# Optimization experiments

Measured on AMD Instinct MI355X. Metric: run time of the kernel, lower is better.

The kernel has to match this reference:

```python
import jax, jax.numpy as jnp
import numpy as np

B, T, L = 32, 512, 16   # clips, transitions per clip, IMU samples per transition
C_IN = 6
H1, H2, H3 = 64, 128, 256
OUT = 256
EPS = 1e-5
SLOPE = 0.1


def setup_inputs() -> dict:
    key = jax.random.key(0)
    ks = jax.random.split(key, 24)
    f32 = jnp.float32

    def n(k, shape, s=0.05):
        return jax.random.normal(k, shape, f32) * s

    inp = {
        "imu": jax.random.normal(ks[0], (B, T, L, C_IN), f32),
        # conv block 1
        "w1": n(ks[1], (H1, C_IN, 3)), "b1": n(ks[2], (H1,)),
        "g1": 1.0 + n(ks[3], (H1,)), "be1": n(ks[4], (H1,)),
        "m1": n(ks[5], (H1,)), "v1": jax.random.uniform(ks[6], (H1,), f32, 0.5, 1.5),
        # conv block 2
        "w2": n(ks[7], (H2, H1, 3)), "b2": n(ks[8], (H2,)),
        "g2": 1.0 + n(ks[9], (H2,)), "be2": n(ks[10], (H2,)),
        "m2": n(ks[11], (H2,)), "v2": jax.random.uniform(ks[12], (H2,), f32, 0.5, 1.5),
        # conv block 3
        "w3": n(ks[13], (H3, H2, 3)), "b3": n(ks[14], (H3,)),
        "g3": 1.0 + n(ks[15], (H3,)), "be3": n(ks[16], (H3,)),
        "m3": n(ks[17], (H3,)), "v3": jax.random.uniform(ks[18], (H3,), f32, 0.5, 1.5),
        # projection (torch Linear: y = x @ W.T + b)
        "wp": n(ks[19], (OUT, H3)), "bp": n(ks[20], (OUT,)),
    }
    return inp


def _conv1d(x, w, b):
    # x: [N, C, L], w: [O, I, K], 'same' padding=1 for K=3
    y = jax.lax.conv_general_dilated(
        x, w, window_strides=(1,), padding=[(1, 1)],
        dimension_numbers=("NCH", "OIH", "NCH"))
    return y + b[None, :, None]


def _block(x, w, b, g, be, m, v):
    # Conv1d -> BatchNorm1d (eval, running stats) -> LeakyReLU(0.1); dropout = identity (eval)
    y = _conv1d(x, w, b)
    y = g[None, :, None] * (y - m[None, :, None]) * jax.lax.rsqrt(v + EPS)[None, :, None] + be[None, :, None]
    return jnp.where(y > 0, y, SLOPE * y)


def reference(imu, w1, b1, g1, be1, m1, v1,
              w2, b2, g2, be2, m2, v2,
              w3, b3, g3, be3, m3, v3,
              wp, bp):
    # Flatten the (batch, transition) double loop into one batched pipeline.
    # imu: [B, T, L, 6] -> [B*T, 6, L]  (= .transpose(0,1).unsqueeze(0) per segment)
    x = imu.reshape(B * T, L, C_IN).transpose(0, 2, 1)
    x = _block(x, w1, b1, g1, be1, m1, v1)
    x = _block(x, w2, b2, g2, be2, m2, v2)
    x = _block(x, w3, b3, g3, be3, m3, v3)   # [B*T, 256, L]
    x = jnp.mean(x, axis=-1)                  # AdaptiveAvgPool1d(1) -> [B*T, 256]
    out = x @ wp.T + bp                       # projection -> [B*T, 256]
    return out.reshape(B, T, OUT)
```

## Files before the change

kernel.cpp:

```cpp
#include <hip/hip_runtime.h>
#include <cstdint>
#include <cstddef>


namespace {

typedef __attribute__((ext_vector_type(8))) short short8;
typedef __attribute__((ext_vector_type(4))) float f32x4;

constexpr int NSEG = 32 * 512;
constexpr float kEps = 1e-5f;

constexpr size_t OFF_A2F = 0;
constexpr size_t OFF_A3F = 49152;
constexpr size_t OFF_WP  = 245760;
constexpr size_t OFF_B2  = 376832;
constexpr size_t OFF_B3  = 377344;
constexpr size_t OFF_A1F = 378368;
constexpr size_t OFF_B1C = 382464;
constexpr size_t WS_NEED = 382720;

constexpr int L_ACT2 = 20736;
constexpr int L_IMC  = 59904;
constexpr int L_POOL = 70144;
constexpr int L_TOTAL = 78592;

__device__ __forceinline__ unsigned short f2bf(float f) {
    union { float f; unsigned int u; } a; a.f = f;
    unsigned int u = a.u + 0x7FFFu + ((a.u >> 16) & 1u);
    return (unsigned short)(u >> 16);
}

__device__ __forceinline__ unsigned int cvt_pk_bf16(float a, float b) {
    unsigned int r;
    asm("v_cvt_pk_bf16_f32 %0, %1, %2" : "=v"(r) : "v"(a), "v"(b));
    return r;
}
__device__ __forceinline__ float asf(unsigned int u) {
    union { unsigned int u; float f; } a; a.u = u; return a.f;
}

__device__ __forceinline__ void gll16(const void* g, void* l) {
    __builtin_amdgcn_global_load_lds(
        (const __attribute__((address_space(1))) unsigned int*)g,
        (__attribute__((address_space(3))) unsigned int*)l, 16, 0, 0);
}

__device__ __forceinline__ short8 frag16(const void* p) {
    return __builtin_bit_cast(short8, *(const int4*)p);
}

__device__ __forceinline__ void sync_lds() {
    asm volatile("s_waitcnt lgkmcnt(0)" ::: "memory");
    __builtin_amdgcn_s_barrier();
    asm volatile("" ::: "memory");
    __builtin_amdgcn_sched_barrier(0);
}
__device__ __forceinline__ void sync_vm_lds() {
    asm volatile("s_waitcnt vmcnt(0) lgkmcnt(0)" ::: "memory");
    __builtin_amdgcn_s_barrier();
    asm volatile("" ::: "memory");
    __builtin_amdgcn_sched_barrier(0);
}

__device__ __forceinline__ float leaky(float y) { return fmaxf(y, 0.1f * y); }

__global__ __launch_bounds__(256) void k0_prep(
    const float* __restrict__ w1, const float* __restrict__ b1, const float* __restrict__ g1,
    const float* __restrict__ be1, const float* __restrict__ m1, const float* __restrict__ v1,
    const float* __restrict__ w2, const float* __restrict__ b2, const float* __restrict__ g2,
    const float* __restrict__ be2, const float* __restrict__ m2, const float* __restrict__ v2,
    const float* __restrict__ w3, const float* __restrict__ b3, const float* __restrict__ g3,
    const float* __restrict__ be3, const float* __restrict__ m3, const float* __restrict__ v3,
    const float* __restrict__ wp, char* __restrict__ ws)
{
    int idx = blockIdx.x * 256 + threadIdx.x;
    if (idx < 3072) {
        int f = idx >> 6, lane = idx & 63;
        int tap = f >> 4, qq = (f >> 3) & 1, rtile = f & 7;
        int row = rtile * 16 + (lane & 15);
        int kb = qq * 32 + (lane >> 4) * 8;
        float a = g2[row] * rsqrtf(v2[row] + kEps);
        unsigned short us[8];
#pragma unroll
        for (int j = 0; j < 8; ++j)
            us[j] = f2bf(a * w2[row * 192 + (kb + j) * 3 + tap]);
        *(int4*)(ws + OFF_A2F + (size_t)idx * 16) = *(const int4*)us;
    } else if (idx < 15360) {
        int u = idx - 3072;
        int f = u >> 6, lane = u & 63;
        int ks = f >> 5, qq = (f >> 4) & 1, rtile = f & 15;
        int tap = ks >> 1, ih = ks & 1;
        int row = rtile * 16 + (lane & 15);
        int kb = qq * 32 + (lane >> 4) * 8;
        float a = g3[row] * rsqrtf(v3[row] + kEps);
        unsigned short us[8];
#pragma unroll
        for (int j = 0; j < 8; ++j) {
            int i = ih * 64 + kb + j;
            us[j] = f2bf(a * w3[row * 384 + i * 3 + tap]);
        }
        *(int4*)(ws + OFF_A3F + (size_t)u * 16) = *(const int4*)us;
    } else if (idx < 23552) {
        int u = idx - 15360;
        int f = u >> 6, lane = u & 63;
        int o = (f >> 3) * 16 + (lane & 15);
        int cb = (f & 7) * 32 + (lane >> 4) * 8;
        unsigned short us[8];
#pragma unroll
        for (int j = 0; j < 8; ++j)
            us[j] = f2bf(wp[o * 256 + cb + j] * 0.0625f);
        *(int4*)(ws + OFF_WP + (size_t)u * 16) = *(const int4*)us;
    } else if (idx < 23680) {
        int o = idx - 23552;
        float a = g2[o] * rsqrtf(v2[o] + kEps);
        ((float*)(ws + OFF_B2))[o] = a * (b2[o] - m2[o]) + be2[o];
    } else if (idx < 23936) {
        int o = idx - 23680;
        float a = g3[o] * rsqrtf(v3[o] + kEps);
        ((float*)(ws + OFF_B3))[o] = a * (b3[o] - m3[o]) + be3[o];
    } else if (idx < 24192) {
        int u = idx - 23936;
        int f = u >> 6, lane = u & 63;
        int row = f * 16 + (lane & 15);
        float a = g1[row] * rsqrtf(v1[row] + kEps);
        unsigned short us[8];
#pragma unroll
        for (int j = 0; j < 8; ++j) {
            int k = (lane >> 4) * 8 + j;
            us[j] = (k < 18) ? f2bf(a * w1[row * 18 + k]) : (unsigned short)0;
        }
        *(int4*)(ws + OFF_A1F + (size_t)u * 16) = *(const int4*)us;
    } else if (idx < 24256) {
        int o = idx - 24192;
        float a = g1[o] * rsqrtf(v1[o] + kEps);
        ((float*)(ws + OFF_B1C))[o] = a * (b1[o] - m1[o]) + be1[o];
    }
}

__global__ __launch_bounds__(512, 4) void k_all(
    const float* __restrict__ imu,
    const char* __restrict__ ws, const float* __restrict__ bp,
    float* __restrict__ out)
{
    __shared__ char smem[L_TOTAL];
    char* act1L  = smem;
    char* act2L  = smem + L_ACT2;
    char* imcL   = smem + L_IMC;
    char* poolsL = smem + L_POOL;
    char* imuL   = poolsL;
    const char* A2F = ws + OFF_A2F;
    const char* A3F = ws + OFF_A3F;
    const char* WPF = ws + OFF_WP;
    const float* bias2 = (const float*)(ws + OFF_B2);
    const float* bias3 = (const float*)(ws + OFF_B3);

    const int tid = threadIdx.x, lane = tid & 63, wid = tid >> 6;
    const int lo = lane & 15, hi = lane >> 4;
    const int seg0 = blockIdx.x * 8;

    short8 a1p[4];
#pragma unroll
    for (int m = 0; m < 4; ++m)
        a1p[m] = frag16(ws + OFF_A1F + (size_t)(m * 64 + lane) * 16);
    float4 bb4[4];
#pragma unroll
    for (int m = 0; m < 4; ++m)
        bb4[m] = *(const float4*)((const float*)(ws + OFF_B1C) + m * 16 + hi * 4);

    if (wid < 3)
        gll16((const char*)imu + (size_t)seg0 * 384 + wid * 1024 + lane * 16,
              imuL + wid * 1024);
    sync_vm_lds();

    {
        const float* xf = (const float*)imuL;
        const int kq = wid & 3;
        const int col = (wid >> 2) * 64 + lane;
        const int seg = col >> 4, l = col & 15;
        const float* xb = xf + seg * 96 + l * 6;
        float v[8];
        if (kq == 0) {
            v[0] = l > 0  ? xb[-6] : 0.f;
            v[1] = xb[0];
            v[2] = l < 15 ? xb[6]  : 0.f;
            v[3] = l > 0  ? xb[-5] : 0.f;
            v[4] = xb[1];
            v[5] = l < 15 ? xb[7]  : 0.f;
            v[6] = l > 0  ? xb[-4] : 0.f;
            v[7] = xb[2];
        } else if (kq == 1) {
            v[0] = l < 15 ? xb[8]  : 0.f;
            v[1] = l > 0  ? xb[-3] : 0.f;
            v[2] = xb[3];
            v[3] = l < 15 ? xb[9]  : 0.f;
            v[4] = l > 0  ? xb[-2] : 0.f;
            v[5] = xb[4];
            v[6] = l < 15 ? xb[10] : 0.f;
            v[7] = l > 0  ? xb[-1] : 0.f;
        } else if (kq == 2) {
            v[0] = xb[5];
            v[1] = l < 15 ? xb[11] : 0.f;
            v[2] = v[3] = v[4] = v[5] = v[6] = v[7] = 0.f;
        } else {
            v[0] = v[1] = v[2] = v[3] = v[4] = v[5] = v[6] = v[7] = 0.f;
        }
        uint4 pk;
        pk.x = cvt_pk_bf16(v[0], v[1]);
        pk.y = cvt_pk_bf16(v[2], v[3]);
        pk.z = cvt_pk_bf16(v[4], v[5]);
        pk.w = cvt_pk_bf16(v[6], v[7]);
        *(uint4*)(imcL + seg * 1280 + l * 80 + kq * 16) = pk;

        if (tid < 144) {
            int s = tid / 18, rest = tid % 18;
            int h = rest / 9, unit = rest % 9;
            int4 z; z.x = z.y = z.z = z.w = 0;
            *(int4*)(act1L + (s * 18 + h * 17) * 144 + unit * 16) = z;
        }
        if (tid < 272) {
            int s = tid / 34, rest = tid % 34;
            int h = rest / 17, unit = rest % 17;
            int4 z; z.x = z.y = z.z = z.w = 0;
            *(int4*)(act2L + (s * 18 + h * 17) * 272 + unit * 16) = z;
        }
    }
    sync_lds();

    {
        f32x4 acc1[4];
#pragma unroll
        for (int m = 0; m < 4; ++m) acc1[m] = f32x4{0.f, 0.f, 0.f, 0.f};
        short8 bq = frag16(imcL + wid * 1280 + lo * 80 + hi * 16);
        __builtin_amdgcn_s_setprio(1);
#pragma unroll
        for (int m = 0; m < 4; ++m)
            acc1[m] = __builtin_amdgcn_mfma_f32_16x16x32_bf16(a1p[m], bq, acc1[m], 0, 0, 0);
        __builtin_amdgcn_s_setprio(0);
#pragma unroll
        for (int m = 0; m < 4; ++m) {
            float y0 = leaky(acc1[m][0] + bb4[m].x);
            float y1 = leaky(acc1[m][1] + bb4[m].y);
            float y2 = leaky(acc1[m][2] + bb4[m].z);
            float y3 = leaky(acc1[m][3] + bb4[m].w);
            uint2 pk;
            pk.x = cvt_pk_bf16(y0, y1);
            pk.y = cvt_pk_bf16(y2, y3);
            *(uint2*)(act1L + (wid * 18 + lo + 1) * 144 + m * 32 + hi * 8) = pk;
        }
    }

    const int mi2 = wid >> 1, ni2 = wid & 1;
    short8 a2p[2][2];
#pragma unroll
    for (int s = 0; s < 2; ++s)
#pragma unroll
        for (int rt = 0; rt < 2; ++rt)
            a2p[s][rt] = frag16(A2F + (size_t)((s * 8 + mi2 * 2 + rt) * 64 + lane) * 16);

    sync_lds();

    f32x4 acc2[2][4];
#pragma unroll
    for (int i = 0; i < 2; ++i)
#pragma unroll
        for (int j = 0; j < 4; ++j) acc2[i][j] = f32x4{0.f, 0.f, 0.f, 0.f};
    {
        const char* b1base = act1L + lo * 144 + hi * 16;
#pragma unroll
        for (int s = 0; s < 6; ++s) {
            const int tap = s >> 1, qq = s & 1;
            short8 bfr[4];
#pragma unroll
            for (int ct = 0; ct < 4; ++ct)
                bfr[ct] = frag16(b1base + ((ni2 * 4 + ct) * 18 + tap) * 144 + qq * 64);
            __builtin_amdgcn_s_setprio(1);
#pragma unroll
            for (int ct = 0; ct < 4; ++ct) {
                acc2[0][ct] = __builtin_amdgcn_mfma_f32_16x16x32_bf16(a2p[s & 1][0], bfr[ct], acc2[0][ct], 0, 0, 0);
                acc2[1][ct] = __builtin_amdgcn_mfma_f32_16x16x32_bf16(a2p[s & 1][1], bfr[ct], acc2[1][ct], 0, 0, 0);
            }
            __builtin_amdgcn_s_setprio(0);
            if (s < 4) {
#pragma unroll
                for (int rt = 0; rt < 2; ++rt)
                    a2p[s & 1][rt] = frag16(A2F + (size_t)(((s + 2) * 8 + mi2 * 2 + rt) * 64 + lane) * 16);
            }
        }
    }

    const int ni3 = wid >> 1, mi3 = wid & 1;
    short8 w3p[2][4];
#pragma unroll
    for (int s = 0; s < 2; ++s)
#pragma unroll
        for (int ct = 0; ct < 4; ++ct)
            w3p[s][ct] = frag16(A3F + (size_t)((s * 16 + ni3 * 4 + ct) * 64 + lane) * 16);
    float b3r[4];
#pragma unroll
    for (int ct = 0; ct < 4; ++ct)
        b3r[ct] = bias3[(ni3 * 4 + ct) * 16 + lo];

#pragma unroll
    for (int rt = 0; rt < 2; ++rt) {
        int ch0 = (mi2 * 2 + rt) * 16 + hi * 4;
        float4 b4 = *(const float4*)(bias2 + ch0);
#pragma unroll
        for (int ct = 0; ct < 4; ++ct) {
            float y0 = leaky(acc2[rt][ct][0] + b4.x);
            float y1 = leaky(acc2[rt][ct][1] + b4.y);
            float y2 = leaky(acc2[rt][ct][2] + b4.z);
            float y3 = leaky(acc2[rt][ct][3] + b4.w);
            uint2 pk;
            pk.x = cvt_pk_bf16(y0, y1);
            pk.y = cvt_pk_bf16(y2, y3);
            *(uint2*)(act2L + ((ni2 * 4 + ct) * 18 + lo + 1) * 272 + ch0 * 2) = pk;
        }
    }
    sync_lds();

    f32x4 acc3[4][4];
#pragma unroll
    for (int i = 0; i < 4; ++i)
#pragma unroll
        for (int j = 0; j < 4; ++j) acc3[i][j] = f32x4{0.f, 0.f, 0.f, 0.f};
    {
#pragma unroll
        for (int s = 0; s < 12; ++s) {
            const int tap = s >> 2, ih = (s >> 1) & 1, qq = s & 1;
            short8 afr[4];
#pragma unroll
            for (int mt = 0; mt < 4; ++mt)
                afr[mt] = frag16(act2L + ((mi3 * 4 + mt) * 18 + lo + tap) * 272
                                 + ih * 128 + qq * 64 + hi * 16);
            __builtin_amdgcn_s_setprio(1);
#pragma unroll
            for (int mt = 0; mt < 4; ++mt)
#pragma unroll
                for (int ct = 0; ct < 4; ++ct)
                    acc3[mt][ct] = __builtin_amdgcn_mfma_f32_16x16x32_bf16(
                        afr[mt], w3p[s & 1][ct], acc3[mt][ct], 0, 0, 0);
            __builtin_amdgcn_s_setprio(0);
            if (s < 10) {
#pragma unroll
                for (int ct = 0; ct < 4; ++ct)
                    w3p[s & 1][ct] = frag16(A3F + (size_t)(((s + 2) * 16 + ni3 * 4 + ct) * 64 + lane) * 16);
            }
        }
    }

#pragma unroll
    for (int ct = 0; ct < 4; ++ct) {
        int co = (ni3 * 4 + ct) * 16 + lo;
        float bv = b3r[ct];
        float t[4];
#pragma unroll
        for (int mt = 0; mt < 4; ++mt) {
            float s4 = 0.f;
#pragma unroll
            for (int r = 0; r < 4; ++r)
                s4 += leaky(acc3[mt][ct][r] + bv);
            s4 += __shfl_xor(s4, 16, 64);
            s4 += __shfl_xor(s4, 32, 64);
            t[mt] = s4;
        }
        unsigned int pkA = cvt_pk_bf16(t[0], t[1]);
        unsigned int pkB = cvt_pk_bf16(t[2], t[3]);
        float r0 = t[0] - asf(pkA << 16);
        float r1 = t[1] - asf(pkA & 0xffff0000u);
        float r2 = t[2] - asf(pkB << 16);
        float r3 = t[3] - asf(pkB & 0xffff0000u);
        unsigned int pkrA = cvt_pk_bf16(r0, r1);
        unsigned int pkrB = cvt_pk_bf16(r2, r3);
        if (hi == 0) {
            int row0 = mi3 * 4;
            char* pc = poolsL + co * 2;
            *(unsigned short*)(pc + (row0 + 0) * 528) = (unsigned short)pkA;
            *(unsigned short*)(pc + (row0 + 1) * 528) = (unsigned short)(pkA >> 16);
            *(unsigned short*)(pc + (row0 + 2) * 528) = (unsigned short)pkB;
            *(unsigned short*)(pc + (row0 + 3) * 528) = (unsigned short)(pkB >> 16);
            *(unsigned short*)(pc + (row0 + 8) * 528) = (unsigned short)pkrA;
            *(unsigned short*)(pc + (row0 + 9) * 528) = (unsigned short)(pkrA >> 16);
            *(unsigned short*)(pc + (row0 + 10) * 528) = (unsigned short)pkrB;
            *(unsigned short*)(pc + (row0 + 11) * 528) = (unsigned short)(pkrB >> 16);
        }
    }

    short8 wbp[2][2];
#pragma unroll
    for (int q = 0; q < 2; ++q)
#pragma unroll
        for (int ct = 0; ct < 2; ++ct)
            wbp[q][ct] = frag16(WPF + (size_t)(((wid * 2 + ct) * 8 + q) * 64 + lane) * 16);

    sync_lds();

    {
        f32x4 acc4[2];
        acc4[0] = f32x4{0.f, 0.f, 0.f, 0.f};
        acc4[1] = f32x4{0.f, 0.f, 0.f, 0.f};
#pragma unroll
        for (int q = 0; q < 8; ++q) {
            short8 pa = frag16(poolsL + lo * 528 + q * 64 + hi * 16);
            acc4[0] = __builtin_amdgcn_mfma_f32_16x16x32_bf16(pa, wbp[q & 1][0], acc4[0], 0, 0, 0);
            acc4[1] = __builtin_amdgcn_mfma_f32_16x16x32_bf16(pa, wbp[q & 1][1], acc4[1], 0, 0, 0);
            if (q < 6) {
#pragma unroll
                for (int ct = 0; ct < 2; ++ct)
                    wbp[q & 1][ct] = frag16(WPF + (size_t)(((wid * 2 + ct) * 8 + q + 2) * 64 + lane) * 16);
            }
        }
#pragma unroll
        for (int ct = 0; ct < 2; ++ct) {
            int o = (wid * 2 + ct) * 16 + lo;
            float bv = bp[o];
#pragma unroll
            for (int r = 0; r < 4; ++r) {
                float t = acc4[ct][r] + __shfl_xor(acc4[ct][r], 32, 64);
                if (hi < 2)
                    out[(size_t)(seg0 + hi * 4 + r) * 256 + o] = t + bv;
            }
        }
    }
}

}

extern "C" void kernel_launch(void* const* d_in, const int* in_sizes, int n_in,
                              void* d_out, int out_size, void* d_ws, size_t ws_size,
                              hipStream_t stream) {
    if (ws_size < WS_NEED) return;

    const float* imu = (const float*)d_in[0];
    const float* w1 = (const float*)d_in[1];  const float* b1 = (const float*)d_in[2];
    const float* g1 = (const float*)d_in[3];  const float* be1 = (const float*)d_in[4];
    const float* m1 = (const float*)d_in[5];  const float* v1 = (const float*)d_in[6];
    const float* w2 = (const float*)d_in[7];  const float* b2 = (const float*)d_in[8];
    const float* g2 = (const float*)d_in[9];  const float* be2 = (const float*)d_in[10];
    const float* m2 = (const float*)d_in[11]; const float* v2 = (const float*)d_in[12];
    const float* w3 = (const float*)d_in[13]; const float* b3 = (const float*)d_in[14];
    const float* g3 = (const float*)d_in[15]; const float* be3 = (const float*)d_in[16];
    const float* m3 = (const float*)d_in[17]; const float* v3 = (const float*)d_in[18];
    const float* wp = (const float*)d_in[19]; const float* bp = (const float*)d_in[20];
    float* out = (float*)d_out;
    char* ws = (char*)d_ws;

    hipLaunchKernelGGL(k0_prep, dim3(95), dim3(256), 0, stream,
                       w1, b1, g1, be1, m1, v1,
                       w2, b2, g2, be2, m2, v2, w3, b3, g3, be3, m3, v3, wp, ws);
    hipLaunchKernelGGL(k_all, dim3(NSEG / 8), dim3(512), 0, stream,
                       imu, ws, bp, out);
}
```

Before: 82.03 us.

## Switch layer-3 conv GEMM to 32x32x16 MFMA with re-tiled weight fragments

Layer 3 moves from 16x16x32 bf16 MFMAs to 32x32x16 bf16 MFMAs. The layer-3 weight prepack layout is rearranged to match, and the wave-to-tile mapping becomes two segments by 128 output channels per wave. This cuts the number of LDS activation fragment loads per MFMA and issues fewer, larger matrix instructions, aiming at higher matrix-core throughput. In exchange, the accumulators move into 16-wide vectors, which may change register pressure, and the pooling epilogue and its LDS writes are rewritten for the new accumulator layout.

```diff
diff --git a/kernel.cpp b/kernel.cpp
--- a/kernel.cpp
+++ b/kernel.cpp
@@ -7,6 +7,7 @@
 
 typedef __attribute__((ext_vector_type(8))) short short8;
 typedef __attribute__((ext_vector_type(4))) float f32x4;
+typedef __attribute__((ext_vector_type(16))) float f32x16;
 
 constexpr int NSEG = 32 * 512;
 constexpr float kEps = 1e-5f;
@@ -89,16 +90,16 @@
     } else if (idx < 15360) {
         int u = idx - 3072;
         int f = u >> 6, lane = u & 63;
-        int ks = f >> 5, qq = (f >> 4) & 1, rtile = f & 15;
-        int tap = ks >> 1, ih = ks & 1;
-        int row = rtile * 16 + (lane & 15);
-        int kb = qq * 32 + (lane >> 4) * 8;
-        float a = g3[row] * rsqrtf(v3[row] + kEps);
+        int ks = f >> 3, ctile = f & 7;
+        int tap = ks >> 3;
+        int cout = ctile * 32 + (lane & 31);
+        int klocal = (lane >> 5) * 8;
+        float a = g3[cout] * rsqrtf(v3[cout] + kEps);
         unsigned short us[8];
 #pragma unroll
         for (int j = 0; j < 8; ++j) {
-            int i = ih * 64 + kb + j;
-            us[j] = f2bf(a * w3[row * 384 + i * 3 + tap]);
+            int i = (ks & 7) * 16 + klocal + j;
+            us[j] = f2bf(a * w3[cout * 384 + i * 3 + tap]);
         }
         *(int4*)(ws + OFF_A3F + (size_t)u * 16) = *(const int4*)us;
     } else if (idx < 23552) {
@@ -289,17 +290,18 @@
         }
     }
 
-    const int ni3 = wid >> 1, mi3 = wid & 1;
+    const int s0 = 2 * (wid & 3);
+    const int cb32 = (wid >> 2) * 4;
     short8 w3p[2][4];
 #pragma unroll
     for (int s = 0; s < 2; ++s)
 #pragma unroll
         for (int ct = 0; ct < 4; ++ct)
-            w3p[s][ct] = frag16(A3F + (size_t)((s * 16 + ni3 * 4 + ct) * 64 + lane) * 16);
+            w3p[s][ct] = frag16(A3F + (size_t)((s * 8 + cb32 + ct) * 64 + lane) * 16);
     float b3r[4];
 #pragma unroll
     for (int ct = 0; ct < 4; ++ct)
-        b3r[ct] = bias3[(ni3 * 4 + ct) * 16 + lo];
+        b3r[ct] = bias3[(cb32 + ct) * 32 + (lane & 31)];
 
 #pragma unroll
     for (int rt = 0; rt < 2; ++rt) {
@@ -319,70 +321,56 @@
     }
     sync_lds();
 
-    f32x4 acc3[4][4];
-#pragma unroll
-    for (int i = 0; i < 4; ++i)
-#pragma unroll
-        for (int j = 0; j < 4; ++j) acc3[i][j] = f32x4{0.f, 0.f, 0.f, 0.f};
+    f32x16 acc3v[4];
+#pragma unroll
+    for (int t = 0; t < 4; ++t)
+#pragma unroll
+        for (int r = 0; r < 16; ++r) acc3v[t][r] = 0.f;
     {
-#pragma unroll
-        for (int s = 0; s < 12; ++s) {
-            const int tap = s >> 2, ih = (s >> 1) & 1, qq = s & 1;
-            short8 afr[4];
-#pragma unroll
-            for (int mt = 0; mt < 4; ++mt)
-                afr[mt] = frag16(act2L + ((mi3 * 4 + mt) * 18 + lo + tap) * 272
-                                 + ih * 128 + qq * 64 + hi * 16);
+        const int arow = lane & 31;
+        const char* a3base = act2L + ((s0 + (arow >> 4)) * 18 + (arow & 15)) * 272
+                             + (lane >> 5) * 16;
+#pragma unroll
+        for (int ks = 0; ks < 24; ++ks) {
+            const int tap = ks >> 3, kc = ks & 7;
+            short8 afr = frag16(a3base + tap * 272 + kc * 32);
             __builtin_amdgcn_s_setprio(1);
 #pragma unroll
-            for (int mt = 0; mt < 4; ++mt)
+            for (int t = 0; t < 4; ++t)
+                acc3v[t] = __builtin_amdgcn_mfma_f32_32x32x16_bf16(
+                    afr, w3p[ks & 1][t], acc3v[t], 0, 0, 0);
+            __builtin_amdgcn_s_setprio(0);
+            if (ks < 22) {
 #pragma unroll
                 for (int ct = 0; ct < 4; ++ct)
-                    acc3[mt][ct] = __builtin_amdgcn_mfma_f32_16x16x32_bf16(
-                        afr[mt], w3p[s & 1][ct], acc3[mt][ct], 0, 0, 0);
-            __builtin_amdgcn_s_setprio(0);
-            if (s < 10) {
-#pragma unroll
-                for (int ct = 0; ct < 4; ++ct)
-                    w3p[s & 1][ct] = frag16(A3F + (size_t)(((s + 2) * 16 + ni3 * 4 + ct) * 64 + lane) * 16);
+                    w3p[ks & 1][ct] = frag16(A3F + (size_t)(((ks + 2) * 8 + cb32 + ct) * 64 + lane) * 16);
             }
         }
     }
 
 #pragma unroll
-    for (int ct = 0; ct < 4; ++ct) {
-        int co = (ni3 * 4 + ct) * 16 + lo;
-        float bv = b3r[ct];
-        float t[4];
-#pragma unroll
-        for (int mt = 0; mt < 4; ++mt) {
-            float s4 = 0.f;
-#pragma unroll
-            for (int r = 0; r < 4; ++r)
-                s4 += leaky(acc3[mt][ct][r] + bv);
-            s4 += __shfl_xor(s4, 16, 64);
-            s4 += __shfl_xor(s4, 32, 64);
-            t[mt] = s4;
-        }
-        unsigned int pkA = cvt_pk_bf16(t[0], t[1]);
-        unsigned int pkB = cvt_pk_bf16(t[2], t[3]);
-        float r0 = t[0] - asf(pkA << 16);
-        float r1 = t[1] - asf(pkA & 0xffff0000u);
-        float r2 = t[2] - asf(pkB << 16);
-        float r3 = t[3] - asf(pkB & 0xffff0000u);
-        unsigned int pkrA = cvt_pk_bf16(r0, r1);
-        unsigned int pkrB = cvt_pk_bf16(r2, r3);
-        if (hi == 0) {
-            int row0 = mi3 * 4;
-            char* pc = poolsL + co * 2;
-            *(unsigned short*)(pc + (row0 + 0) * 528) = (unsigned short)pkA;
-            *(unsigned short*)(pc + (row0 + 1) * 528) = (unsigned short)(pkA >> 16);
-            *(unsigned short*)(pc + (row0 + 2) * 528) = (unsigned short)pkB;
-            *(unsigned short*)(pc + (row0 + 3) * 528) = (unsigned short)(pkB >> 16);
-            *(unsigned short*)(pc + (row0 + 8) * 528) = (unsigned short)pkrA;
-            *(unsigned short*)(pc + (row0 + 9) * 528) = (unsigned short)(pkrA >> 16);
-            *(unsigned short*)(pc + (row0 + 10) * 528) = (unsigned short)pkrB;
-            *(unsigned short*)(pc + (row0 + 11) * 528) = (unsigned short)(pkrB >> 16);
+    for (int t = 0; t < 4; ++t) {
+        float bv = b3r[t];
+        float sA = 0.f, sB = 0.f;
+#pragma unroll
+        for (int r = 0; r < 8; ++r)
+            sA += leaky(acc3v[t][r] + bv);
+#pragma unroll
+        for (int r = 8; r < 16; ++r)
+            sB += leaky(acc3v[t][r] + bv);
+        sA += __shfl_xor(sA, 32, 64);
+        sB += __shfl_xor(sB, 32, 64);
+        unsigned int pk = cvt_pk_bf16(sA, sB);
+        float rA = sA - asf(pk << 16);
+        float rB = sB - asf(pk & 0xffff0000u);
+        unsigned int pkr = cvt_pk_bf16(rA, rB);
+        if (lane < 32) {
+            int cout = (cb32 + t) * 32 + lane;
+            char* pc = poolsL + cout * 2;
+            *(unsigned short*)(pc + (s0 + 0) * 528) = (unsigned short)pk;
+            *(unsigned short*)(pc + (s0 + 1) * 528) = (unsigned short)(pk >> 16);
+            *(unsigned short*)(pc + (s0 + 8) * 528) = (unsigned short)pkr;
+            *(unsigned short*)(pc + (s0 + 9) * 528) = (unsigned short)(pkr >> 16);
         }
     }
 
```

Result: slower. 88.37 us (+7.7%).

## Build layer-1 im2col fragments in registers and drop staging barriers

Applied to the files above, without the earlier changes.

Each wave now loads its own segment's IMU data into a private LDS slice and waits only on its own vector loads, with no block barrier. It then builds the layer-1 MFMA B-fragment directly in registers instead of staging an im2col buffer in LDS. This removes two block-wide barriers and one LDS round trip, and frees about 10 KB of LDS per block. The s_setprio hints around the MFMA loops are also removed. The halo zeroing of act1/act2 moves after layer 1, and the LDS region holding the raw IMU data is reused for pooling later, so correctness depends on the remaining barrier ordering.

```diff
diff --git a/kernel.cpp b/kernel.cpp
--- a/kernel.cpp
+++ b/kernel.cpp
@@ -21,9 +21,8 @@
 constexpr size_t WS_NEED = 382720;
 
 constexpr int L_ACT2 = 20736;
-constexpr int L_IMC  = 59904;
-constexpr int L_POOL = 70144;
-constexpr int L_TOTAL = 78592;
+constexpr int L_POOL = 59904;
+constexpr int L_TOTAL = 68352;
 
 __device__ __forceinline__ unsigned short f2bf(float f) {
     union { float f; unsigned int u; } a; a.f = f;
@@ -52,12 +51,6 @@
 
 __device__ __forceinline__ void sync_lds() {
     asm volatile("s_waitcnt lgkmcnt(0)" ::: "memory");
-    __builtin_amdgcn_s_barrier();
-    asm volatile("" ::: "memory");
-    __builtin_amdgcn_sched_barrier(0);
-}
-__device__ __forceinline__ void sync_vm_lds() {
-    asm volatile("s_waitcnt vmcnt(0) lgkmcnt(0)" ::: "memory");
     __builtin_amdgcn_s_barrier();
     asm volatile("" ::: "memory");
     __builtin_amdgcn_sched_barrier(0);
@@ -146,7 +139,6 @@
     __shared__ char smem[L_TOTAL];
     char* act1L  = smem;
     char* act2L  = smem + L_ACT2;
-    char* imcL   = smem + L_IMC;
     char* poolsL = smem + L_POOL;
     char* imuL   = poolsL;
     const char* A2F = ws + OFF_A2F;
@@ -168,75 +160,53 @@
     for (int m = 0; m < 4; ++m)
         bb4[m] = *(const float4*)((const float*)(ws + OFF_B1C) + m * 16 + hi * 4);
 
-    if (wid < 3)
-        gll16((const char*)imu + (size_t)seg0 * 384 + wid * 1024 + lane * 16,
-              imuL + wid * 1024);
-    sync_vm_lds();
+    if (lane < 24)
+        gll16((const char*)imu + (size_t)(seg0 + wid) * 384 + lane * 16,
+              imuL + wid * 384);
+    asm volatile("s_waitcnt vmcnt(0)" ::: "memory");
+    __builtin_amdgcn_sched_barrier(0);
 
     {
-        const float* xf = (const float*)imuL;
-        const int kq = wid & 3;
-        const int col = (wid >> 2) * 64 + lane;
-        const int seg = col >> 4, l = col & 15;
-        const float* xb = xf + seg * 96 + l * 6;
+        const float* xb = (const float*)(imuL + wid * 384) + lo * 6;
         float v[8];
-        if (kq == 0) {
-            v[0] = l > 0  ? xb[-6] : 0.f;
+        if (hi == 0) {
+            v[0] = lo > 0  ? xb[-6] : 0.f;
             v[1] = xb[0];
-            v[2] = l < 15 ? xb[6]  : 0.f;
-            v[3] = l > 0  ? xb[-5] : 0.f;
+            v[2] = lo < 15 ? xb[6]  : 0.f;
+            v[3] = lo > 0  ? xb[-5] : 0.f;
             v[4] = xb[1];
-            v[5] = l < 15 ? xb[7]  : 0.f;
-            v[6] = l > 0  ? xb[-4] : 0.f;
+            v[5] = lo < 15 ? xb[7]  : 0.f;
+            v[6] = lo > 0  ? xb[-4] : 0.f;
             v[7] = xb[2];
-        } else if (kq == 1) {
-            v[0] = l < 15 ? xb[8]  : 0.f;
-            v[1] = l > 0  ? xb[-3] : 0.f;
+        } else if (hi == 1) {
+            v[0] = lo < 15 ? xb[8]  : 0.f;
+            v[1] = lo > 0  ? xb[-3] : 0.f;
             v[2] = xb[3];
-            v[3] = l < 15 ? xb[9]  : 0.f;
-            v[4] = l > 0  ? xb[-2] : 0.f;
+            v[3] = lo < 15 ? xb[9]  : 0.f;
+            v[4] = lo > 0  ? xb[-2] : 0.f;
             v[5] = xb[4];
-            v[6] = l < 15 ? xb[10] : 0.f;
-            v[7] = l > 0  ? xb[-1] : 0.f;
-        } else if (kq == 2) {
+            v[6] = lo < 15 ? xb[10] : 0.f;
+            v[7] = lo > 0  ? xb[-1] : 0.f;
+        } else if (hi == 2) {
             v[0] = xb[5];
-            v[1] = l < 15 ? xb[11] : 0.f;
+            v[1] = lo < 15 ? xb[11] : 0.f;
             v[2] = v[3] = v[4] = v[5] = v[6] = v[7] = 0.f;
         } else {
             v[0] = v[1] = v[2] = v[3] = v[4] = v[5] = v[6] = v[7] = 0.f;
         }
-        uint4 pk;
-        pk.x = cvt_pk_bf16(v[0], v[1]);
-        pk.y = cvt_pk_bf16(v[2], v[3]);
-        pk.z = cvt_pk_bf16(v[4], v[5]);
-        pk.w = cvt_pk_bf16(v[6], v[7]);
-        *(uint4*)(imcL + seg * 1280 + l * 80 + kq * 16) = pk;
-
-        if (tid < 144) {
-            int s = tid / 18, rest = tid % 18;
-            int h = rest / 9, unit = rest % 9;
-            int4 z; z.x = z.y = z.z = z.w = 0;
-            *(int4*)(act1L + (s * 18 + h * 17) * 144 + unit * 16) = z;
-        }
-        if (tid < 272) {
-            int s = tid / 34, rest = tid % 34;
-            int h = rest / 17, unit = rest % 17;
-            int4 z; z.x = z.y = z.z = z.w = 0;
-            *(int4*)(act2L + (s * 18 + h * 17) * 272 + unit * 16) = z;
-        }
-    }
-    sync_lds();
-
-    {
+        uint4 pkv;
+        pkv.x = cvt_pk_bf16(v[0], v[1]);
+        pkv.y = cvt_pk_bf16(v[2], v[3]);
+        pkv.z = cvt_pk_bf16(v[4], v[5]);
+        pkv.w = cvt_pk_bf16(v[6], v[7]);
+        short8 bq = __builtin_bit_cast(short8, pkv);
+
         f32x4 acc1[4];
 #pragma unroll
         for (int m = 0; m < 4; ++m) acc1[m] = f32x4{0.f, 0.f, 0.f, 0.f};
-        short8 bq = frag16(imcL + wid * 1280 + lo * 80 + hi * 16);
-        __builtin_amdgcn_s_setprio(1);
 #pragma unroll
         for (int m = 0; m < 4; ++m)
             acc1[m] = __builtin_amdgcn_mfma_f32_16x16x32_bf16(a1p[m], bq, acc1[m], 0, 0, 0);
-        __builtin_amdgcn_s_setprio(0);
 #pragma unroll
         for (int m = 0; m < 4; ++m) {
             float y0 = leaky(acc1[m][0] + bb4[m].x);
@@ -248,6 +218,18 @@
             pk.y = cvt_pk_bf16(y2, y3);
             *(uint2*)(act1L + (wid * 18 + lo + 1) * 144 + m * 32 + hi * 8) = pk;
         }
+        if (tid < 144) {
+            int s = tid / 18, rest = tid % 18;
+            int h = rest / 9, unit = rest % 9;
+            int4 z; z.x = z.y = z.z = z.w = 0;
+            *(int4*)(act1L + (s * 18 + h * 17) * 144 + unit * 16) = z;
+        }
+        if (tid < 272) {
+            int s = tid / 34, rest = tid % 34;
+            int h = rest / 17, unit = rest % 17;
+            int4 z; z.x = z.y = z.z = z.w = 0;
+            *(int4*)(act2L + (s * 18 + h * 17) * 272 + unit * 16) = z;
+        }
     }
 
     const int mi2 = wid >> 1, ni2 = wid & 1;
@@ -274,13 +256,11 @@
 #pragma unroll
             for (int ct = 0; ct < 4; ++ct)
                 bfr[ct] = frag16(b1base + ((ni2 * 4 + ct) * 18 + tap) * 144 + qq * 64);
-            __builtin_amdgcn_s_setprio(1);
 #pragma unroll
             for (int ct = 0; ct < 4; ++ct) {
                 acc2[0][ct] = __builtin_amdgcn_mfma_f32_16x16x32_bf16(a2p[s & 1][0], bfr[ct], acc2[0][ct], 0, 0, 0);
                 acc2[1][ct] = __builtin_amdgcn_mfma_f32_16x16x32_bf16(a2p[s & 1][1], bfr[ct], acc2[1][ct], 0, 0, 0);
             }
-            __builtin_amdgcn_s_setprio(0);
             if (s < 4) {
 #pragma unroll
                 for (int rt = 0; rt < 2; ++rt)
@@ -333,14 +313,12 @@
             for (int mt = 0; mt < 4; ++mt)
                 afr[mt] = frag16(act2L + ((mi3 * 4 + mt) * 18 + lo + tap) * 272
                                  + ih * 128 + qq * 64 + hi * 16);
-            __builtin_amdgcn_s_setprio(1);
 #pragma unroll
             for (int mt = 0; mt < 4; ++mt)
 #pragma unroll
                 for (int ct = 0; ct < 4; ++ct)
                     acc3[mt][ct] = __builtin_amdgcn_mfma_f32_16x16x32_bf16(
                         afr[mt], w3p[s & 1][ct], acc3[mt][ct], 0, 0, 0);
-            __builtin_amdgcn_s_setprio(0);
             if (s < 10) {
 #pragma unroll
                 for (int ct = 0; ct < 4; ++ct)
```

Result: no change. 80.92 us (-1.4%).
